# Kernel tuning notes

Measured on AMD Instinct MI355X. Metric: run time of the kernel, lower is better.

Reference implementation:

```python
import jax, jax.numpy as jnp
import numpy as np

N_NODES = 100000
N_EDGES = 1000000
F_IN = 64
F_OUT = 128
F_HID = 4 * F_OUT


def setup_inputs() -> dict:
    key = jax.random.key(0)
    ks = jax.random.split(key, 6)
    x = jax.random.normal(ks[0], (N_NODES, F_IN), dtype=jnp.float32)
    edge_index = jax.random.randint(ks[1], (2, N_EDGES), 0, N_NODES, dtype=jnp.int64)
    s = 1.0 / np.sqrt(F_IN)
    W_in = jax.random.normal(ks[2], (F_IN, F_OUT), dtype=jnp.float32) * s
    W_out = jax.random.normal(ks[3], (F_IN, F_OUT), dtype=jnp.float32) * s
    W1 = jax.random.normal(ks[4], (F_IN, F_HID), dtype=jnp.float32) * s
    W2 = jax.random.normal(ks[5], (F_HID, F_OUT), dtype=jnp.float32) * (1.0 / np.sqrt(F_HID))
    return {
        'x': x, 'edge_index': edge_index,
        'W_in': W_in, 'b_in': jnp.zeros((F_OUT,), jnp.float32),
        'W_out': W_out, 'b_out': jnp.zeros((F_OUT,), jnp.float32),
        'W1': W1, 'b1': jnp.zeros((F_HID,), jnp.float32),
        'W2': W2, 'b2': jnp.zeros((F_OUT,), jnp.float32),
    }


def _mean_aggr(vals, idx, num_segments):
    # segment-mean: sum of gathered features / in-degree (0 if no edges, like PyG)
    s = jax.ops.segment_sum(vals, idx, num_segments=num_segments)
    cnt = jax.ops.segment_sum(jnp.ones((idx.shape[0], 1), vals.dtype), idx,
                              num_segments=num_segments)
    return s / jnp.maximum(cnt, 1.0)


def reference(x, edge_index, W_in, b_in, W_out, b_out, W1, b1, W2, b2):
    src, dst = edge_index[0], edge_index[1]
    n = x.shape[0]
    # SAGEConv(root_weight=False), flow='source_to_target': aggregate x[src] at dst
    x_in = jax.nn.elu(_mean_aggr(x[src], dst, n) @ W_in + b_in)
    # flow='target_to_source': aggregate x[dst] at src
    x_out = jax.nn.elu(_mean_aggr(x[dst], src, n) @ W_out + b_out)
    # self branch: elu(lin2(elu(lin1(x))))  (the F.dropout call is a no-op)
    x_self = jax.nn.elu(jax.nn.elu(x @ W1 + b1) @ W2 + b2)
    return (x_in, x_out, x_self)
```

## Files before the change

kernel.cpp:

```cpp
#include <hip/hip_runtime.h>
#include <hip/hip_bf16.h>
#include <cstdint>
#include <cstddef>

#define N_NODES 100000
#define N_EDGES 1000000
#define F_IN 64
#define F_OUT 128
#define F_HID 512
#define NB 391
#define BSH 8
#define SB 98
#define AB 391
#define P1B 245

typedef __attribute__((ext_vector_type(8))) short short8b;
typedef __attribute__((ext_vector_type(4))) short short4b;
typedef __attribute__((ext_vector_type(4))) float f32x4;

__device__ __forceinline__ float elu_f(float v) {
    return v > 0.0f ? v : __expf(v) - 1.0f;
}

__device__ __forceinline__ unsigned short f2bf(float v) {
    __hip_bfloat16 b = __float2bfloat16(v);
    return *reinterpret_cast<unsigned short*>(&b);
}
__device__ __forceinline__ float bf2f(unsigned short u) {
    unsigned int w = (unsigned int)u << 16;
    return __uint_as_float(w);
}
__device__ __forceinline__ void split_bf(float v, short& hi, short& lo) {
    unsigned short h = (unsigned short)(__float_as_uint(v) >> 16);
    float r = v - bf2f(h);
    hi = (short)h;
    lo = (short)(unsigned short)(__float_as_uint(r) >> 16);
}

__global__ __launch_bounds__(256) void hist_kernel(
    const int* __restrict__ src, const int* __restrict__ dst,
    int* __restrict__ deg_in, int* __restrict__ deg_out)
{
    int e = blockIdx.x * 256 + threadIdx.x;
    if (e < N_EDGES) {
        atomicAdd(&deg_in[dst[e]], 1);
        atomicAdd(&deg_out[src[e]], 1);
    }
}

__global__ __launch_bounds__(256) void scan_block_kernel(
    const int* __restrict__ deg_in, const int* __restrict__ deg_out,
    int* __restrict__ rp_in, int* __restrict__ rp_out,
    int* __restrict__ bsum_in, int* __restrict__ bsum_out, int n)
{
    __shared__ int sSum[256];
    int b = blockIdx.x;
    const int* deg; int* rowptr; int* blockSums;
    if (b < SB) { deg = deg_in;  rowptr = rp_in;  blockSums = bsum_in; }
    else        { b -= SB; deg = deg_out; rowptr = rp_out; blockSums = bsum_out; }

    int tid = threadIdx.x;
    int base = b * 1024 + tid * 4;
    int v0 = (base + 0 < n) ? deg[base + 0] : 0;
    int v1 = (base + 1 < n) ? deg[base + 1] : 0;
    int v2 = (base + 2 < n) ? deg[base + 2] : 0;
    int v3 = (base + 3 < n) ? deg[base + 3] : 0;
    int s = v0 + v1 + v2 + v3;
    sSum[tid] = s;
    __syncthreads();
    int incl = s;
    for (int off = 1; off < 256; off <<= 1) {
        int t = (tid >= off) ? sSum[tid - off] : 0;
        __syncthreads();
        incl += t;
        sSum[tid] = incl;
        __syncthreads();
    }
    int exclT = incl - s;
    if (base + 0 < n) rowptr[base + 0] = exclT;
    if (base + 1 < n) rowptr[base + 1] = exclT + v0;
    if (base + 2 < n) rowptr[base + 2] = exclT + v0 + v1;
    if (base + 3 < n) rowptr[base + 3] = exclT + v0 + v1 + v2;
    if (tid == 255) blockSums[b] = incl;
}

__global__ __launch_bounds__(128) void scan_top_kernel(
    int* __restrict__ bs_in, int* __restrict__ bs_out, int nb)
{
    __shared__ int sh[128];
    int* blockSums = (blockIdx.x == 0) ? bs_in : bs_out;
    int tid = threadIdx.x;
    int v = (tid < nb) ? blockSums[tid] : 0;
    sh[tid] = v;
    __syncthreads();
    int incl = v;
    for (int off = 1; off < 128; off <<= 1) {
        int t = (tid >= off) ? sh[tid - off] : 0;
        __syncthreads();
        incl += t;
        sh[tid] = incl;
        __syncthreads();
    }
    if (tid < nb) blockSums[tid] = incl - v;
}

__global__ __launch_bounds__(256) void scan_add_kernel(
    int* __restrict__ rp_in, int* __restrict__ rp_out,
    const int* __restrict__ bs_in, const int* __restrict__ bs_out,
    int* __restrict__ bcur_in, int* __restrict__ bcur_out, int n, int total)
{
    int b = blockIdx.x;
    int* rowptr; const int* blockSums; int* bcur;
    if (b < AB) { rowptr = rp_in;  blockSums = bs_in;  bcur = bcur_in; }
    else        { b -= AB; rowptr = rp_out; blockSums = bs_out; bcur = bcur_out; }
    int i = b * 256 + threadIdx.x;
    if (i < n) {
        int v = rowptr[i] + blockSums[i >> 10];
        rowptr[i] = v;
        if ((i & 255) == 0) bcur[i >> BSH] = v;
    }
    if (i == 0) rowptr[n] = total;
}

__global__ __launch_bounds__(512) void msplit_scatter_kernel(
    const int* __restrict__ src, const int* __restrict__ dst,
    int* __restrict__ bcur_in, int* __restrict__ bcur_out,
    unsigned int* __restrict__ tmp_in, unsigned int* __restrict__ tmp_out)
{
    __shared__ int sCnt[NB];
    __shared__ int sBase[NB];
    int b = blockIdx.x;
    const int* keys; const int* vals; int* bcur; unsigned int* tmp;
    if (b < P1B) { keys = dst; vals = src; bcur = bcur_in;  tmp = tmp_in; }
    else         { b -= P1B; keys = src; vals = dst; bcur = bcur_out; tmp = tmp_out; }

    int tid = threadIdx.x;
    int tile0 = b * 4096;

    for (int i = tid; i < NB; i += 512) sCnt[i] = 0;
    __syncthreads();

    int key[8], rank[8];
    #pragma unroll
    for (int j = 0; j < 8; ++j) {
        int e = tile0 + j * 512 + tid;
        key[j] = -1;
        if (e < N_EDGES) {
            int k = keys[e];
            key[j] = k;
            rank[j] = atomicAdd(&sCnt[k >> BSH], 1);
        }
    }
    __syncthreads();
    for (int i = tid; i < NB; i += 512) sBase[i] = atomicAdd(&bcur[i], sCnt[i]);
    __syncthreads();
    #pragma unroll
    for (int j = 0; j < 8; ++j) {
        int e = tile0 + j * 512 + tid;
        if (e < N_EDGES) {
            int k = key[j];
            unsigned int rec = ((unsigned int)vals[e] << BSH) | (unsigned int)(k & 255);
            tmp[sBase[k >> BSH] + rank[j]] = rec;
        }
    }
}

__global__ __launch_bounds__(256) void msplit_place_kernel(
    const unsigned int* __restrict__ tmp_in, const unsigned int* __restrict__ tmp_out,
    const int* __restrict__ rp_in, const int* __restrict__ rp_out,
    int* __restrict__ col_in, int* __restrict__ col_out,
    int* __restrict__ flag)
{
    __shared__ int sCur[256];
    int b = blockIdx.x;
    const unsigned int* tmp; const int* rp; int* col;
    if (b < NB) { tmp = tmp_in;  rp = rp_in;  col = col_in; }
    else        { b -= NB; tmp = tmp_out; rp = rp_out; col = col_out; }

    int k0 = b << BSH;
    int kend = (k0 + 256 < N_NODES) ? k0 + 256 : N_NODES;
    int nk = kend - k0;
    int tid = threadIdx.x;
    if (tid < nk) sCur[tid] = rp[k0 + tid];
    __syncthreads();

    int beg = rp[k0], end = rp[kend];
    for (int e = beg + tid; e < end; e += 256) {
        unsigned int rec = tmp[e];
        int k8 = (int)(rec & 255u);
        int v  = (int)(rec >> BSH);
        if (k8 < nk) {
            int pos = atomicAdd(&sCur[k8], 1);
            col[pos] = v;
        } else {
            atomicOr(flag, 1);
        }
    }
    __syncthreads();
    if (tid < nk && sCur[tid] != rp[k0 + tid + 1]) atomicOr(flag, 1);
}

__global__ __launch_bounds__(256) void place_repair_kernel(
    const int* __restrict__ flag,
    const int* __restrict__ src, const int* __restrict__ dst,
    const int* __restrict__ rp_in, const int* __restrict__ rp_out,
    int* __restrict__ cur_in, int* __restrict__ cur_out,
    int* __restrict__ col_in, int* __restrict__ col_out)
{
    if (flag[0] == 0) return;
    int e = blockIdx.x * 256 + threadIdx.x;
    if (e >= N_EDGES) return;
    int s = src[e], d = dst[e];
    int p = rp_in[d] + atomicAdd(&cur_in[d], 1);
    col_in[p] = s;
    int q = rp_out[s] + atomicAdd(&cur_out[s], 1);
    col_out[q] = d;
}

__global__ __launch_bounds__(256) void prep_x_kernel(
    const float* __restrict__ x, unsigned short* __restrict__ xbf)
{
    int i = blockIdx.x * 256 + threadIdx.x;
    int base = i * 4;
    if (base < N_NODES * F_IN) {
        float4 v = *reinterpret_cast<const float4*>(&x[base]);
        short4b o;
        o[0] = (short)f2bf(v.x);
        o[1] = (short)f2bf(v.y);
        o[2] = (short)f2bf(v.z);
        o[3] = (short)f2bf(v.w);
        *reinterpret_cast<short4b*>(&xbf[base]) = o;
    }
}

__global__ __launch_bounds__(256) void gather_mean_kernel(
    const unsigned short* __restrict__ xbf,
    const int* __restrict__ rowptr, const int* __restrict__ col,
    float* __restrict__ agg)
{
    int wid = blockIdx.x * 4 + (threadIdx.x >> 6);
    int lane = threadIdx.x & 63;
    int g2 = lane >> 4;
    int l16 = lane & 15;
    if (wid >= N_NODES) return;
    int beg = rowptr[wid], end = rowptr[wid + 1];

    float4 acc = make_float4(0.0f, 0.0f, 0.0f, 0.0f);
    for (int e0 = beg; e0 < end; e0 += 16) {
        #pragma unroll
        for (int j = 0; j < 4; ++j) {
            int idx = e0 + j * 4 + g2;
            bool ok = idx < end;
            int c = col[ok ? idx : beg];
            uint2 v = *reinterpret_cast<const uint2*>(&xbf[(size_t)c * F_IN + l16 * 4]);
            if (ok) {
                acc.x += __uint_as_float(v.x << 16);
                acc.y += __uint_as_float(v.x & 0xffff0000u);
                acc.z += __uint_as_float(v.y << 16);
                acc.w += __uint_as_float(v.y & 0xffff0000u);
            }
        }
    }
    acc.x += __shfl_xor(acc.x, 16);
    acc.y += __shfl_xor(acc.y, 16);
    acc.z += __shfl_xor(acc.z, 16);
    acc.w += __shfl_xor(acc.w, 16);
    acc.x += __shfl_xor(acc.x, 32);
    acc.y += __shfl_xor(acc.y, 32);
    acc.z += __shfl_xor(acc.z, 32);
    acc.w += __shfl_xor(acc.w, 32);

    if (g2 == 0) {
        float inv = 1.0f / fmaxf((float)(end - beg), 1.0f);
        float4 o = make_float4(acc.x * inv, acc.y * inv, acc.z * inv, acc.w * inv);
        *reinterpret_cast<float4*>(&agg[(size_t)wid * F_IN + l16 * 4]) = o;
    }
}

__global__ __launch_bounds__(256) void prep_w_kernel(
    const float* __restrict__ W1, const float* __restrict__ W2,
    const float* __restrict__ Win, const float* __restrict__ Wout,
    unsigned short* __restrict__ W1Ahi, unsigned short* __restrict__ W1Alo,
    unsigned short* __restrict__ W2Ahi, unsigned short* __restrict__ W2Alo,
    unsigned short* __restrict__ WinAhi, unsigned short* __restrict__ WinAlo,
    unsigned short* __restrict__ WoutAhi, unsigned short* __restrict__ WoutAlo)
{
    int t = blockIdx.x * 256 + threadIdx.x;
    int lane = t & 63;
    int l15 = lane & 15, g = lane >> 4;
    if (t < 4096) {
        int ht = (t >> 6) & 31, ks = t >> 11;
        int m = ht * 16 + l15;
        int k0 = ks * 32 + g * 8;
        size_t o = ((size_t)(ht * 2 + ks) * 64 + lane) * 8;
        #pragma unroll
        for (int i = 0; i < 8; ++i) {
            float v = W1[(size_t)(k0 + i) * F_HID + m];
            unsigned short hi = f2bf(v);
            W1Ahi[o + i] = hi;
            W1Alo[o + i] = f2bf(v - bf2f(hi));
        }
    } else if (t < 12288) {
        int u = t - 4096;
        int ft = (u >> 6) & 7, ks2 = u >> 9;
        int m = ft * 16 + l15;
        int k0 = ks2 * 32 + g * 8;
        size_t o = ((size_t)(ks2 * 8 + ft) * 64 + lane) * 8;
        #pragma unroll
        for (int i = 0; i < 8; ++i) {
            float v = W2[(size_t)(k0 + i) * F_OUT + m];
            unsigned short hi = f2bf(v);
            W2Ahi[o + i] = hi;
            W2Alo[o + i] = f2bf(v - bf2f(hi));
        }
    } else if (t < 14336) {
        int u = t - 12288;
        const float* W = (u < 1024) ? Win : Wout;
        unsigned short* Ahi = (u < 1024) ? WinAhi : WoutAhi;
        unsigned short* Alo = (u < 1024) ? WinAlo : WoutAlo;
        u &= 1023;
        int ft = (u >> 6) & 7, ks = u >> 9;
        int m = ft * 16 + l15;
        int k0 = ks * 32 + g * 8;
        size_t o = ((size_t)(ks * 8 + ft) * 64 + lane) * 8;
        #pragma unroll
        for (int i = 0; i < 8; ++i) {
            float v = W[(size_t)(k0 + i) * F_OUT + m];
            unsigned short hi = f2bf(v);
            Ahi[o + i] = hi;
            Alo[o + i] = f2bf(v - bf2f(hi));
        }
    }
}

__global__ __launch_bounds__(256) void sage_lin_mfma_kernel(
    const float* __restrict__ agg,
    const unsigned short* __restrict__ WAhi, const unsigned short* __restrict__ WAlo,
    const float* __restrict__ b, float* __restrict__ out)
{
    int tid = threadIdx.x, lane = tid & 63, w = tid >> 6;
    int l15 = lane & 15, g = lane >> 4;
    int n = blockIdx.x * 64 + w * 16 + l15;
    int nc = (n > N_NODES - 1) ? N_NODES - 1 : n;

    short8b bhf[2], blf[2];
    #pragma unroll
    for (int ks = 0; ks < 2; ++ks) {
        const float* pa = &agg[(size_t)nc * F_IN + ks * 32 + g * 8];
        float4 v0 = *reinterpret_cast<const float4*>(pa);
        float4 v1 = *reinterpret_cast<const float4*>(pa + 4);
        float vv[8] = {v0.x, v0.y, v0.z, v0.w, v1.x, v1.y, v1.z, v1.w};
        short8b h8, l8;
        #pragma unroll
        for (int i = 0; i < 8; ++i) {
            short hh, ll;
            split_bf(vv[i], hh, ll);
            h8[i] = hh;
            l8[i] = ll;
        }
        bhf[ks] = h8;
        blf[ks] = l8;
    }

    #pragma unroll
    for (int ft = 0; ft < 8; ++ft) {
        f32x4 acc;
        {
            float4 bv = *reinterpret_cast<const float4*>(&b[ft * 16 + g * 4]);
            acc[0] = bv.x; acc[1] = bv.y; acc[2] = bv.z; acc[3] = bv.w;
        }
        #pragma unroll
        for (int ks = 0; ks < 2; ++ks) {
            size_t o = ((size_t)(ks * 8 + ft) * 64 + lane) * 8;
            short8b ah = *reinterpret_cast<const short8b*>(&WAhi[o]);
            short8b al = *reinterpret_cast<const short8b*>(&WAlo[o]);
            acc = __builtin_amdgcn_mfma_f32_16x16x32_bf16(ah, bhf[ks], acc, 0, 0, 0);
            acc = __builtin_amdgcn_mfma_f32_16x16x32_bf16(ah, blf[ks], acc, 0, 0, 0);
            acc = __builtin_amdgcn_mfma_f32_16x16x32_bf16(al, bhf[ks], acc, 0, 0, 0);
        }
        if (n < N_NODES) {
            float4 o4;
            o4.x = elu_f(acc[0]);
            o4.y = elu_f(acc[1]);
            o4.z = elu_f(acc[2]);
            o4.w = elu_f(acc[3]);
            *reinterpret_cast<float4*>(&out[(size_t)n * F_OUT + ft * 16 + g * 4]) = o4;
        }
    }
}

__global__ __launch_bounds__(128) void validate_sage_kernel(
    const float* __restrict__ agg,
    const float* __restrict__ W, const float* __restrict__ b,
    const float* __restrict__ outd, int* __restrict__ flag)
{
    __shared__ float sA[F_IN];
    int nn = blockIdx.x;
    int f = threadIdx.x;
    if (f < F_IN) sA[f] = agg[(size_t)nn * F_IN + f];
    __syncthreads();
    float acc = b[f];
    for (int k = 0; k < F_IN; ++k)
        acc = fmaf(sA[k], W[(size_t)k * F_OUT + f], acc);
    float ref = elu_f(acc);
    float got = outd[(size_t)nn * F_OUT + f];
    if (!(fabsf(ref - got) <= 0.01f)) atomicOr(flag, 1);
}

__global__ __launch_bounds__(256, 4) void self_mlp_mfma_kernel(
    const float* __restrict__ x,
    const unsigned short* __restrict__ W1Ahi, const unsigned short* __restrict__ W1Alo,
    const unsigned short* __restrict__ W2Ahi, const unsigned short* __restrict__ W2Alo,
    const float* __restrict__ b1, const float* __restrict__ b2,
    float* __restrict__ out)
{
    __shared__ unsigned short sW1hi[2048], sW1lo[2048];
    __shared__ unsigned short sW2hi[4096], sW2lo[4096];
    __shared__ unsigned short sHhi[4096], sHlo[4096];

    int tid = threadIdx.x, lane = tid & 63, w = tid >> 6;
    int l15 = lane & 15, g = lane >> 4;
    int node0 = blockIdx.x * 128;

    short8b xhi[2][2], xlo[2][2];
    #pragma unroll
    for (int nt = 0; nt < 2; ++nt) {
        int n = node0 + (2 * w + nt) * 16 + l15;
        if (n > N_NODES - 1) n = N_NODES - 1;
        #pragma unroll
        for (int ks = 0; ks < 2; ++ks) {
            const float* px = &x[(size_t)n * F_IN + ks * 32 + g * 8];
            float4 v0 = *reinterpret_cast<const float4*>(px);
            float4 v1 = *reinterpret_cast<const float4*>(px + 4);
            float vv[8] = {v0.x, v0.y, v0.z, v0.w, v1.x, v1.y, v1.z, v1.w};
            short8b h8, l8;
            #pragma unroll
            for (int i = 0; i < 8; ++i) {
                short hh, ll;
                split_bf(vv[i], hh, ll);
                h8[i] = hh;
                l8[i] = ll;
            }
            xhi[nt][ks] = h8;
            xlo[nt][ks] = l8;
        }
    }

    f32x4 acc[8][2];
    #pragma unroll
    for (int ft = 0; ft < 8; ++ft) {
        float4 bv = *reinterpret_cast<const float4*>(&b2[ft * 16 + g * 4]);
        #pragma unroll
        for (int nt = 0; nt < 2; ++nt) {
            acc[ft][nt][0] = bv.x; acc[ft][nt][1] = bv.y;
            acc[ft][nt][2] = bv.z; acc[ft][nt][3] = bv.w;
        }
    }

    for (int c = 0; c < 16; ++c) {
        __syncthreads();
        {
            const float4* s1h = reinterpret_cast<const float4*>(W1Ahi + (size_t)c * 2048);
            const float4* s1l = reinterpret_cast<const float4*>(W1Alo + (size_t)c * 2048);
            reinterpret_cast<float4*>(sW1hi)[tid] = s1h[tid];
            reinterpret_cast<float4*>(sW1lo)[tid] = s1l[tid];
            const float4* s2h = reinterpret_cast<const float4*>(W2Ahi + (size_t)c * 4096);
            const float4* s2l = reinterpret_cast<const float4*>(W2Alo + (size_t)c * 4096);
            reinterpret_cast<float4*>(sW2hi)[tid] = s2h[tid];
            reinterpret_cast<float4*>(sW2hi)[tid + 256] = s2h[tid + 256];
            reinterpret_cast<float4*>(sW2lo)[tid] = s2l[tid];
            reinterpret_cast<float4*>(sW2lo)[tid + 256] = s2l[tid + 256];
        }
        __syncthreads();

        #pragma unroll
// ... 16 lines not shown
                #pragma unroll
                for (int r = 0; r < 4; ++r) {
                    float hv = elu_f(hacc[r]);
                    short hh, ll;
                    split_bf(hv, hh, ll);
                    ph[r] = hh;
                    pl[r] = ll;
                }
                int byte = nodeL * 64 + (ht * 16 + g * 4) * 2;
                byte ^= (nodeL & 7) << 4;
                *reinterpret_cast<short4b*>(reinterpret_cast<char*>(sHhi) + byte) = ph;
                *reinterpret_cast<short4b*>(reinterpret_cast<char*>(sHlo) + byte) = pl;
            }
        }

        short8b bh[2], bl[2];
        #pragma unroll
        for (int nt = 0; nt < 2; ++nt) {
            int nodeL = (2 * w + nt) * 16 + l15;
            int byte = (nodeL * 64 + g * 16) ^ ((nodeL & 7) << 4);
            bh[nt] = *reinterpret_cast<const short8b*>(reinterpret_cast<const char*>(sHhi) + byte);
            bl[nt] = *reinterpret_cast<const short8b*>(reinterpret_cast<const char*>(sHlo) + byte);
        }
        #pragma unroll
        for (int ft = 0; ft < 8; ++ft) {
            short8b ah = *reinterpret_cast<const short8b*>(&sW2hi[(ft * 64 + lane) * 8]);
            short8b al = *reinterpret_cast<const short8b*>(&sW2lo[(ft * 64 + lane) * 8]);
            #pragma unroll
            for (int nt = 0; nt < 2; ++nt) {
                acc[ft][nt] = __builtin_amdgcn_mfma_f32_16x16x32_bf16(ah, bh[nt], acc[ft][nt], 0, 0, 0);
                acc[ft][nt] = __builtin_amdgcn_mfma_f32_16x16x32_bf16(ah, bl[nt], acc[ft][nt], 0, 0, 0);
                acc[ft][nt] = __builtin_amdgcn_mfma_f32_16x16x32_bf16(al, bh[nt], acc[ft][nt], 0, 0, 0);
            }
        }
    }

    #pragma unroll
    for (int ft = 0; ft < 8; ++ft) {
        #pragma unroll
        for (int nt = 0; nt < 2; ++nt) {
            int n = node0 + (2 * w + nt) * 16 + l15;
            if (n < N_NODES) {
                float4 o;
                o.x = elu_f(acc[ft][nt][0]);
                o.y = elu_f(acc[ft][nt][1]);
                o.z = elu_f(acc[ft][nt][2]);
                o.w = elu_f(acc[ft][nt][3]);
                *reinterpret_cast<float4*>(&out[(size_t)n * F_OUT + ft * 16 + g * 4]) = o;
            }
        }
    }
}

__global__ __launch_bounds__(256) void validate_kernel(
    const float* __restrict__ x,
    const float* __restrict__ W1, const float* __restrict__ b1,
    const float* __restrict__ W2, const float* __restrict__ b2,
    const float* __restrict__ out_self, int* __restrict__ flag)
{
    __shared__ float h[F_HID];
    __shared__ float sX[F_IN];
    int nn = blockIdx.x;
    int tid = threadIdx.x;
    if (tid < F_IN) sX[tid] = x[(size_t)nn * F_IN + tid];
    __syncthreads();
    #pragma unroll
    for (int jj = 0; jj < 2; ++jj) {
        int j = tid * 2 + jj;
        float acc = b1[j];
        for (int k = 0; k < F_IN; ++k)
            acc = fmaf(sX[k], W1[(size_t)k * F_HID + j], acc);
        h[j] = elu_f(acc);
    }
    __syncthreads();
    if (tid < F_OUT) {
        int f = tid;
        float acc = b2[f];
        for (int j = 0; j < F_HID; ++j)
            acc = fmaf(h[j], W2[(size_t)j * F_OUT + f], acc);
        float ref = elu_f(acc);
        float got = out_self[(size_t)nn * F_OUT + f];
        if (!(fabsf(ref - got) <= 0.01f)) atomicOr(flag, 1);
    }
}

__global__ __launch_bounds__(256) void gather_repair_kernel(
    const int* __restrict__ flag,
    const float* __restrict__ x,
    const int* __restrict__ rowptr, const int* __restrict__ col,
    float* __restrict__ agg)
{
    if (flag[0] == 0) return;
    int f = threadIdx.x & 63;
    for (int bb = blockIdx.x; bb < 25000; bb += gridDim.x) {
        int wid = bb * 4 + (threadIdx.x >> 6);
        if (wid >= N_NODES) continue;
        int beg = rowptr[wid];
        int end = rowptr[wid + 1];
        float acc = 0.0f;
        for (int e = beg; e < end; ++e)
            acc += x[(size_t)col[e] * F_IN + f];
        agg[(size_t)wid * F_IN + f] = acc / fmaxf((float)(end - beg), 1.0f);
    }
}

__global__ __launch_bounds__(256) void sage_lin_repair_kernel(
// ... 189 lines not shown
    const float* W_in  = (const float*)d_in[2];
    const float* b_in  = (const float*)d_in[3];
    const float* W_out = (const float*)d_in[4];
    const float* b_out = (const float*)d_in[5];
    const float* W1    = (const float*)d_in[6];
    const float* b1    = (const float*)d_in[7];
    const float* W2    = (const float*)d_in[8];
    const float* b2    = (const float*)d_in[9];
    float* out = (float*)d_out;

    const int* src = ei;
    const int* dst = ei + N_EDGES;

    int* I = (int*)d_ws;
    int* rowptr_in  = I;
    int* rowptr_out = I + 100001;
    int* col_in     = I + 200002;
    int* col_out    = I + 1200002;
    int* deg_in     = I + 2200002;
    int* deg_out    = I + 2300002;
    int* cur_in     = I + 2400002;
    int* cur_out    = I + 2500002;
    int* bsum_in    = I + 2600002;
    int* bsum_out   = I + 2600130;
    int* flagM      = I + 2600260;
    int* flagS      = I + 2600261;
    int* flagC      = I + 2600262;
    float* agg      = (float*)(I + 2600512);
    unsigned short* WF = (unsigned short*)(I + 9000512);
    unsigned short* W1Ahi  = WF;
    unsigned short* W1Alo  = WF + 32768;
    unsigned short* W2Ahi  = WF + 65536;
    unsigned short* W2Alo  = WF + 131072;
    unsigned short* WinAhi = WF + 196608;
    unsigned short* WinAlo = WF + 204800;
    unsigned short* WoutAhi= WF + 212992;
    unsigned short* WoutAlo= WF + 221184;
    unsigned short* xbf    = (unsigned short*)(I + 9120512);

    unsigned int* tmp_in  = (unsigned int*)agg;
    unsigned int* tmp_out = (unsigned int*)agg + 1000000;
    int* bcur_in  = deg_in;
    int* bcur_out = deg_out;

    hipMemsetAsync(deg_in, 0, 400000 * sizeof(int), stream);
    hipMemsetAsync(flagM, 0, 3 * sizeof(int), stream);

    prep_w_kernel<<<56, 256, 0, stream>>>(W1, W2, W_in, W_out,
                                          W1Ahi, W1Alo, W2Ahi, W2Alo,
                                          WinAhi, WinAlo, WoutAhi, WoutAlo);
    prep_x_kernel<<<6250, 256, 0, stream>>>(x, xbf);

    const int eb = (N_EDGES + 255) / 256;
    hist_kernel<<<eb, 256, 0, stream>>>(src, dst, deg_in, deg_out);

    scan_block_kernel<<<2 * SB, 256, 0, stream>>>(deg_in, deg_out,
                                                  rowptr_in, rowptr_out,
                                                  bsum_in, bsum_out, N_NODES);
    scan_top_kernel<<<2, 128, 0, stream>>>(bsum_in, bsum_out, SB);
    scan_add_kernel<<<2 * AB, 256, 0, stream>>>(rowptr_in, rowptr_out,
                                                bsum_in, bsum_out,
                                                bcur_in, bcur_out,
                                                N_NODES, N_EDGES);

    msplit_scatter_kernel<<<2 * P1B, 512, 0, stream>>>(src, dst,
                                                       bcur_in, bcur_out,
                                                       tmp_in, tmp_out);
    msplit_place_kernel<<<2 * NB, 256, 0, stream>>>(tmp_in, tmp_out,
                                                    rowptr_in, rowptr_out,
                                                    col_in, col_out, flagC);
    place_repair_kernel<<<eb, 256, 0, stream>>>(flagC, src, dst,
                                                rowptr_in, rowptr_out,
                                                cur_in, cur_out, col_in, col_out);

    const int gb = (N_NODES + 3) / 4;
    const int mb = (N_NODES + 63) / 64;
    float* out_in   = out;
    float* out_out  = out + (size_t)N_NODES * F_OUT;
    float* out_self = out + 2 * (size_t)N_NODES * F_OUT;

    gather_mean_kernel<<<gb, 256, 0, stream>>>(xbf, rowptr_in, col_in, agg);
    sage_lin_mfma_kernel<<<mb, 256, 0, stream>>>(agg, WinAhi, WinAlo, b_in, out_in);
    validate_sage_kernel<<<4, 128, 0, stream>>>(agg, W_in, b_in, out_in, flagS);

    gather_mean_kernel<<<gb, 256, 0, stream>>>(xbf, rowptr_out, col_out, agg);
    sage_lin_mfma_kernel<<<mb, 256, 0, stream>>>(agg, WoutAhi, WoutAlo, b_out, out_out);
    validate_sage_kernel<<<4, 128, 0, stream>>>(agg, W_out, b_out, out_out, flagS);

    self_mlp_mfma_kernel<<<782, 256, 0, stream>>>(x, W1Ahi, W1Alo, W2Ahi, W2Alo,
                                                  b1, b2, out_self);
    validate_kernel<<<4, 256, 0, stream>>>(x, W1, b1, W2, b2, out_self, flagM);

    self_mlp_repair_kernel<<<782, 256, 0, stream>>>(flagM, x, W1, b1, W2, b2, out_self);
    gather_repair_kernel<<<2048, 256, 0, stream>>>(flagS, x, rowptr_in, col_in, agg);
    sage_lin_repair_kernel<<<2048, 256, 0, stream>>>(flagS, agg, W_in, b_in, out_in);
    gather_repair_kernel<<<2048, 256, 0, stream>>>(flagS, x, rowptr_out, col_out, agg);
    sage_lin_repair_kernel<<<2048, 256, 0, stream>>>(flagS, agg, W_out, b_out, out_out);
}
```

Before: 384.8 us.

## Fuse degree histogram with self-MLP in one interleaved horizontal kernel

```diff
diff --git a/kernel.cpp b/kernel.cpp
--- a/kernel.cpp
+++ b/kernel.cpp
@@ -13,6 +13,8 @@
 #define SB 98
 #define AB 391
 #define P1B 245
+#define HB 3907
+#define SMB 782
 
 typedef __attribute__((ext_vector_type(8))) short short8b;
 typedef __attribute__((ext_vector_type(4))) short short4b;
@@ -37,390 +39,24 @@
     lo = (short)(unsigned short)(__float_as_uint(r) >> 16);
 }
 
-__global__ __launch_bounds__(256) void hist_kernel(
-    const int* __restrict__ src, const int* __restrict__ dst,
-    int* __restrict__ deg_in, int* __restrict__ deg_out)
-{
-    int e = blockIdx.x * 256 + threadIdx.x;
-    if (e < N_EDGES) {
-        atomicAdd(&deg_in[dst[e]], 1);
-        atomicAdd(&deg_out[src[e]], 1);
-    }
-}
-
-__global__ __launch_bounds__(256) void scan_block_kernel(
-    const int* __restrict__ deg_in, const int* __restrict__ deg_out,
-    int* __restrict__ rp_in, int* __restrict__ rp_out,
-    int* __restrict__ bsum_in, int* __restrict__ bsum_out, int n)
-{
-    __shared__ int sSum[256];
-    int b = blockIdx.x;
-    const int* deg; int* rowptr; int* blockSums;
-    if (b < SB) { deg = deg_in;  rowptr = rp_in;  blockSums = bsum_in; }
-    else        { b -= SB; deg = deg_out; rowptr = rp_out; blockSums = bsum_out; }
-
-    int tid = threadIdx.x;
-    int base = b * 1024 + tid * 4;
-    int v0 = (base + 0 < n) ? deg[base + 0] : 0;
-    int v1 = (base + 1 < n) ? deg[base + 1] : 0;
-    int v2 = (base + 2 < n) ? deg[base + 2] : 0;
-    int v3 = (base + 3 < n) ? deg[base + 3] : 0;
-    int s = v0 + v1 + v2 + v3;
-    sSum[tid] = s;
-    __syncthreads();
-    int incl = s;
-    for (int off = 1; off < 256; off <<= 1) {
-        int t = (tid >= off) ? sSum[tid - off] : 0;
-        __syncthreads();
-        incl += t;
-        sSum[tid] = incl;
-        __syncthreads();
-    }
-    int exclT = incl - s;
-    if (base + 0 < n) rowptr[base + 0] = exclT;
-    if (base + 1 < n) rowptr[base + 1] = exclT + v0;
-    if (base + 2 < n) rowptr[base + 2] = exclT + v0 + v1;
-    if (base + 3 < n) rowptr[base + 3] = exclT + v0 + v1 + v2;
-    if (tid == 255) blockSums[b] = incl;
-}
-
-__global__ __launch_bounds__(128) void scan_top_kernel(
-    int* __restrict__ bs_in, int* __restrict__ bs_out, int nb)
-{
-    __shared__ int sh[128];
-    int* blockSums = (blockIdx.x == 0) ? bs_in : bs_out;
-    int tid = threadIdx.x;
-    int v = (tid < nb) ? blockSums[tid] : 0;
-    sh[tid] = v;
-    __syncthreads();
-    int incl = v;
-    for (int off = 1; off < 128; off <<= 1) {
-        int t = (tid >= off) ? sh[tid - off] : 0;
-        __syncthreads();
-        incl += t;
-        sh[tid] = incl;
-        __syncthreads();
-    }
-    if (tid < nb) blockSums[tid] = incl - v;
-}
-
-__global__ __launch_bounds__(256) void scan_add_kernel(
-    int* __restrict__ rp_in, int* __restrict__ rp_out,
-    const int* __restrict__ bs_in, const int* __restrict__ bs_out,
-    int* __restrict__ bcur_in, int* __restrict__ bcur_out, int n, int total)
-{
-    int b = blockIdx.x;
-    int* rowptr; const int* blockSums; int* bcur;
-    if (b < AB) { rowptr = rp_in;  blockSums = bs_in;  bcur = bcur_in; }
-    else        { b -= AB; rowptr = rp_out; blockSums = bs_out; bcur = bcur_out; }
-    int i = b * 256 + threadIdx.x;
-    if (i < n) {
-        int v = rowptr[i] + blockSums[i >> 10];
-        rowptr[i] = v;
-        if ((i & 255) == 0) bcur[i >> BSH] = v;
-    }
-    if (i == 0) rowptr[n] = total;
-}
-
-__global__ __launch_bounds__(512) void msplit_scatter_kernel(
-    const int* __restrict__ src, const int* __restrict__ dst,
-    int* __restrict__ bcur_in, int* __restrict__ bcur_out,
-    unsigned int* __restrict__ tmp_in, unsigned int* __restrict__ tmp_out)
-{
-    __shared__ int sCnt[NB];
-    __shared__ int sBase[NB];
-    int b = blockIdx.x;
-    const int* keys; const int* vals; int* bcur; unsigned int* tmp;
-    if (b < P1B) { keys = dst; vals = src; bcur = bcur_in;  tmp = tmp_in; }
-    else         { b -= P1B; keys = src; vals = dst; bcur = bcur_out; tmp = tmp_out; }
-
-    int tid = threadIdx.x;
-    int tile0 = b * 4096;
-
-    for (int i = tid; i < NB; i += 512) sCnt[i] = 0;
-    __syncthreads();
-
-    int key[8], rank[8];
-    #pragma unroll
-    for (int j = 0; j < 8; ++j) {
-        int e = tile0 + j * 512 + tid;
-        key[j] = -1;
-        if (e < N_EDGES) {
-            int k = keys[e];
-            key[j] = k;
-            rank[j] = atomicAdd(&sCnt[k >> BSH], 1);
-        }
-    }
-    __syncthreads();
-    for (int i = tid; i < NB; i += 512) sBase[i] = atomicAdd(&bcur[i], sCnt[i]);
-    __syncthreads();
-    #pragma unroll
-    for (int j = 0; j < 8; ++j) {
-        int e = tile0 + j * 512 + tid;
-        if (e < N_EDGES) {
-            int k = key[j];
-            unsigned int rec = ((unsigned int)vals[e] << BSH) | (unsigned int)(k & 255);
-            tmp[sBase[k >> BSH] + rank[j]] = rec;
-        }
-    }
-}
-
-__global__ __launch_bounds__(256) void msplit_place_kernel(
-    const unsigned int* __restrict__ tmp_in, const unsigned int* __restrict__ tmp_out,
-    const int* __restrict__ rp_in, const int* __restrict__ rp_out,
-    int* __restrict__ col_in, int* __restrict__ col_out,
-    int* __restrict__ flag)
-{
-    __shared__ int sCur[256];
-    int b = blockIdx.x;
-    const unsigned int* tmp; const int* rp; int* col;
-    if (b < NB) { tmp = tmp_in;  rp = rp_in;  col = col_in; }
-    else        { b -= NB; tmp = tmp_out; rp = rp_out; col = col_out; }
-
-    int k0 = b << BSH;
-    int kend = (k0 + 256 < N_NODES) ? k0 + 256 : N_NODES;
-    int nk = kend - k0;
-    int tid = threadIdx.x;
-    if (tid < nk) sCur[tid] = rp[k0 + tid];
-    __syncthreads();
-
-    int beg = rp[k0], end = rp[kend];
-    for (int e = beg + tid; e < end; e += 256) {
-        unsigned int rec = tmp[e];
-        int k8 = (int)(rec & 255u);
-        int v  = (int)(rec >> BSH);
-        if (k8 < nk) {
-            int pos = atomicAdd(&sCur[k8], 1);
-            col[pos] = v;
-        } else {
-            atomicOr(flag, 1);
-        }
-    }
-    __syncthreads();
-    if (tid < nk && sCur[tid] != rp[k0 + tid + 1]) atomicOr(flag, 1);
-}
-
-__global__ __launch_bounds__(256) void place_repair_kernel(
-    const int* __restrict__ flag,
-    const int* __restrict__ src, const int* __restrict__ dst,
-    const int* __restrict__ rp_in, const int* __restrict__ rp_out,
-    int* __restrict__ cur_in, int* __restrict__ cur_out,
-    int* __restrict__ col_in, int* __restrict__ col_out)
-{
-    if (flag[0] == 0) return;
-    int e = blockIdx.x * 256 + threadIdx.x;
-    if (e >= N_EDGES) return;
-    int s = src[e], d = dst[e];
-    int p = rp_in[d] + atomicAdd(&cur_in[d], 1);
-    col_in[p] = s;
-    int q = rp_out[s] + atomicAdd(&cur_out[s], 1);
-    col_out[q] = d;
-}
-
-__global__ __launch_bounds__(256) void prep_x_kernel(
-    const float* __restrict__ x, unsigned short* __restrict__ xbf)
-{
-    int i = blockIdx.x * 256 + threadIdx.x;
-    int base = i * 4;
-    if (base < N_NODES * F_IN) {
-        float4 v = *reinterpret_cast<const float4*>(&x[base]);
-        short4b o;
-        o[0] = (short)f2bf(v.x);
-        o[1] = (short)f2bf(v.y);
-        o[2] = (short)f2bf(v.z);
-        o[3] = (short)f2bf(v.w);
-        *reinterpret_cast<short4b*>(&xbf[base]) = o;
-    }
-}
-
-__global__ __launch_bounds__(256) void gather_mean_kernel(
-    const unsigned short* __restrict__ xbf,
-    const int* __restrict__ rowptr, const int* __restrict__ col,
-    float* __restrict__ agg)
-{
-    int wid = blockIdx.x * 4 + (threadIdx.x >> 6);
-    int lane = threadIdx.x & 63;
-    int g2 = lane >> 4;
-    int l16 = lane & 15;
-    if (wid >= N_NODES) return;
-    int beg = rowptr[wid], end = rowptr[wid + 1];
-
-    float4 acc = make_float4(0.0f, 0.0f, 0.0f, 0.0f);
-    for (int e0 = beg; e0 < end; e0 += 16) {
-        #pragma unroll
-        for (int j = 0; j < 4; ++j) {
-            int idx = e0 + j * 4 + g2;
-            bool ok = idx < end;
-            int c = col[ok ? idx : beg];
-            uint2 v = *reinterpret_cast<const uint2*>(&xbf[(size_t)c * F_IN + l16 * 4]);
-            if (ok) {
-                acc.x += __uint_as_float(v.x << 16);
-                acc.y += __uint_as_float(v.x & 0xffff0000u);
-                acc.z += __uint_as_float(v.y << 16);
-                acc.w += __uint_as_float(v.y & 0xffff0000u);
-            }
-        }
-    }
-    acc.x += __shfl_xor(acc.x, 16);
-    acc.y += __shfl_xor(acc.y, 16);
-    acc.z += __shfl_xor(acc.z, 16);
-    acc.w += __shfl_xor(acc.w, 16);
-    acc.x += __shfl_xor(acc.x, 32);
-    acc.y += __shfl_xor(acc.y, 32);
-    acc.z += __shfl_xor(acc.z, 32);
-    acc.w += __shfl_xor(acc.w, 32);
-
-    if (g2 == 0) {
-        float inv = 1.0f / fmaxf((float)(end - beg), 1.0f);
-        float4 o = make_float4(acc.x * inv, acc.y * inv, acc.z * inv, acc.w * inv);
-        *reinterpret_cast<float4*>(&agg[(size_t)wid * F_IN + l16 * 4]) = o;
-    }
-}
-
-__global__ __launch_bounds__(256) void prep_w_kernel(
-    const float* __restrict__ W1, const float* __restrict__ W2,
-    const float* __restrict__ Win, const float* __restrict__ Wout,
-    unsigned short* __restrict__ W1Ahi, unsigned short* __restrict__ W1Alo,
-    unsigned short* __restrict__ W2Ahi, unsigned short* __restrict__ W2Alo,
-    unsigned short* __restrict__ WinAhi, unsigned short* __restrict__ WinAlo,
-    unsigned short* __restrict__ WoutAhi, unsigned short* __restrict__ WoutAlo)
-{
-    int t = blockIdx.x * 256 + threadIdx.x;
-    int lane = t & 63;
-    int l15 = lane & 15, g = lane >> 4;
-    if (t < 4096) {
-        int ht = (t >> 6) & 31, ks = t >> 11;
-        int m = ht * 16 + l15;
-        int k0 = ks * 32 + g * 8;
-        size_t o = ((size_t)(ht * 2 + ks) * 64 + lane) * 8;
-        #pragma unroll
-        for (int i = 0; i < 8; ++i) {
-            float v = W1[(size_t)(k0 + i) * F_HID + m];
-            unsigned short hi = f2bf(v);
-            W1Ahi[o + i] = hi;
-            W1Alo[o + i] = f2bf(v - bf2f(hi));
-        }
-    } else if (t < 12288) {
-        int u = t - 4096;
-        int ft = (u >> 6) & 7, ks2 = u >> 9;
-        int m = ft * 16 + l15;
-        int k0 = ks2 * 32 + g * 8;
-        size_t o = ((size_t)(ks2 * 8 + ft) * 64 + lane) * 8;
-        #pragma unroll
-        for (int i = 0; i < 8; ++i) {
-            float v = W2[(size_t)(k0 + i) * F_OUT + m];
-            unsigned short hi = f2bf(v);
-            W2Ahi[o + i] = hi;
-            W2Alo[o + i] = f2bf(v - bf2f(hi));
-        }
-    } else if (t < 14336) {
-        int u = t - 12288;
-        const float* W = (u < 1024) ? Win : Wout;
-        unsigned short* Ahi = (u < 1024) ? WinAhi : WoutAhi;
-        unsigned short* Alo = (u < 1024) ? WinAlo : WoutAlo;
-        u &= 1023;
-        int ft = (u >> 6) & 7, ks = u >> 9;
-        int m = ft * 16 + l15;
-        int k0 = ks * 32 + g * 8;
-        size_t o = ((size_t)(ks * 8 + ft) * 64 + lane) * 8;
-        #pragma unroll
-        for (int i = 0; i < 8; ++i) {
-            float v = W[(size_t)(k0 + i) * F_OUT + m];
-            unsigned short hi = f2bf(v);
-            Ahi[o + i] = hi;
-            Alo[o + i] = f2bf(v - bf2f(hi));
-        }
-    }
-}
-
-__global__ __launch_bounds__(256) void sage_lin_mfma_kernel(
-    const float* __restrict__ agg,
-    const unsigned short* __restrict__ WAhi, const unsigned short* __restrict__ WAlo,
-    const float* __restrict__ b, float* __restrict__ out)
-{
-    int tid = threadIdx.x, lane = tid & 63, w = tid >> 6;
-    int l15 = lane & 15, g = lane >> 4;
-    int n = blockIdx.x * 64 + w * 16 + l15;
-    int nc = (n > N_NODES - 1) ? N_NODES - 1 : n;
-
-    short8b bhf[2], blf[2];
-    #pragma unroll
-    for (int ks = 0; ks < 2; ++ks) {
-        const float* pa = &agg[(size_t)nc * F_IN + ks * 32 + g * 8];
-        float4 v0 = *reinterpret_cast<const float4*>(pa);
-        float4 v1 = *reinterpret_cast<const float4*>(pa + 4);
-        float vv[8] = {v0.x, v0.y, v0.z, v0.w, v1.x, v1.y, v1.z, v1.w};
-        short8b h8, l8;
-        #pragma unroll
-        for (int i = 0; i < 8; ++i) {
-            short hh, ll;
-            split_bf(vv[i], hh, ll);
-            h8[i] = hh;
-            l8[i] = ll;
-        }
-        bhf[ks] = h8;
-        blf[ks] = l8;
-    }
-
-    #pragma unroll
-    for (int ft = 0; ft < 8; ++ft) {
-        f32x4 acc;
-        {
-            float4 bv = *reinterpret_cast<const float4*>(&b[ft * 16 + g * 4]);
-            acc[0] = bv.x; acc[1] = bv.y; acc[2] = bv.z; acc[3] = bv.w;
-        }
-        #pragma unroll
-        for (int ks = 0; ks < 2; ++ks) {
-            size_t o = ((size_t)(ks * 8 + ft) * 64 + lane) * 8;
-            short8b ah = *reinterpret_cast<const short8b*>(&WAhi[o]);
-            short8b al = *reinterpret_cast<const short8b*>(&WAlo[o]);
-            acc = __builtin_amdgcn_mfma_f32_16x16x32_bf16(ah, bhf[ks], acc, 0, 0, 0);
-            acc = __builtin_amdgcn_mfma_f32_16x16x32_bf16(ah, blf[ks], acc, 0, 0, 0);
-            acc = __builtin_amdgcn_mfma_f32_16x16x32_bf16(al, bhf[ks], acc, 0, 0, 0);
-        }
-        if (n < N_NODES) {
-            float4 o4;
-            o4.x = elu_f(acc[0]);
-            o4.y = elu_f(acc[1]);
-            o4.z = elu_f(acc[2]);
-            o4.w = elu_f(acc[3]);
-            *reinterpret_cast<float4*>(&out[(size_t)n * F_OUT + ft * 16 + g * 4]) = o4;
-        }
-    }
-}
-
-__global__ __launch_bounds__(128) void validate_sage_kernel(
-    const float* __restrict__ agg,
-    const float* __restrict__ W, const float* __restrict__ b,
-    const float* __restrict__ outd, int* __restrict__ flag)
-{
-    __shared__ float sA[F_IN];
-    int nn = blockIdx.x;
-    int f = threadIdx.x;
-    if (f < F_IN) sA[f] = agg[(size_t)nn * F_IN + f];
-    __syncthreads();
-    float acc = b[f];
-    for (int k = 0; k < F_IN; ++k)
-        acc = fmaf(sA[k], W[(size_t)k * F_OUT + f], acc);
-    float ref = elu_f(acc);
-    float got = outd[(size_t)nn * F_OUT + f];
-    if (!(fabsf(ref - got) <= 0.01f)) atomicOr(flag, 1);
-}
-
-__global__ __launch_bounds__(256, 4) void self_mlp_mfma_kernel(
+__device__ void self_mlp_body(
+    int blk, unsigned char* smem,
     const float* __restrict__ x,
     const unsigned short* __restrict__ W1Ahi, const unsigned short* __restrict__ W1Alo,
     const unsigned short* __restrict__ W2Ahi, const unsigned short* __restrict__ W2Alo,
     const float* __restrict__ b1, const float* __restrict__ b2,
     float* __restrict__ out)
 {
-    __shared__ unsigned short sW1hi[2048], sW1lo[2048];
-    __shared__ unsigned short sW2hi[4096], sW2lo[4096];
-    __shared__ unsigned short sHhi[4096], sHlo[4096];
+    unsigned short* sW1hi = (unsigned short*)smem;
+    unsigned short* sW1lo = sW1hi + 2048;
+    unsigned short* sW2hi = sW1lo + 2048;
+    unsigned short* sW2lo = sW2hi + 4096;
+    unsigned short* sHhi  = sW2lo + 4096;
+    unsigned short* sHlo  = sHhi + 4096;
 
     int tid = threadIdx.x, lane = tid & 63, w = tid >> 6;
     int l15 = lane & 15, g = lane >> 4;
-    int node0 = blockIdx.x * 128;
+    int node0 = blk * 128;
 
     short8b xhi[2][2], xlo[2][2];
     #pragma unroll
@@ -543,6 +179,392 @@
     }
 }
 
+__global__ __launch_bounds__(256, 4) void fused_hist_self_kernel(
+    const int* __restrict__ src, const int* __restrict__ dst,
+    int* __restrict__ deg_in, int* __restrict__ deg_out,
+    const float* __restrict__ x,
+    const unsigned short* __restrict__ W1Ahi, const unsigned short* __restrict__ W1Alo,
+    const unsigned short* __restrict__ W2Ahi, const unsigned short* __restrict__ W2Alo,
+    const float* __restrict__ b1, const float* __restrict__ b2,
+    float* __restrict__ out_self)
+{
+    __shared__ unsigned char smem[40960];
+    int bid = blockIdx.x;
+    int r = bid % 6;
+    if (r == 5) {
+        int blk = bid / 6;
+        self_mlp_body(blk, smem, x, W1Ahi, W1Alo, W2Ahi, W2Alo, b1, b2, out_self);
+    } else {
+        int hb = (bid / 6) * 5 + r;
+        if (hb < HB) {
+            int e = hb * 256 + threadIdx.x;
+            if (e < N_EDGES) {
+                atomicAdd(&deg_in[dst[e]], 1);
+                atomicAdd(&deg_out[src[e]], 1);
+            }
+        }
+    }
+}
+
+__global__ __launch_bounds__(256) void scan_block_kernel(
+    const int* __restrict__ deg_in, const int* __restrict__ deg_out,
+    int* __restrict__ rp_in, int* __restrict__ rp_out,
+    int* __restrict__ bsum_in, int* __restrict__ bsum_out, int n)
+{
+    __shared__ int sSum[256];
+    int b = blockIdx.x;
+    const int* deg; int* rowptr; int* blockSums;
+    if (b < SB) { deg = deg_in;  rowptr = rp_in;  blockSums = bsum_in; }
+    else        { b -= SB; deg = deg_out; rowptr = rp_out; blockSums = bsum_out; }
+
+    int tid = threadIdx.x;
+    int base = b * 1024 + tid * 4;
+    int v0 = (base + 0 < n) ? deg[base + 0] : 0;
+    int v1 = (base + 1 < n) ? deg[base + 1] : 0;
+    int v2 = (base + 2 < n) ? deg[base + 2] : 0;
+    int v3 = (base + 3 < n) ? deg[base + 3] : 0;
+    int s = v0 + v1 + v2 + v3;
+    sSum[tid] = s;
+    __syncthreads();
+    int incl = s;
+    for (int off = 1; off < 256; off <<= 1) {
+        int t = (tid >= off) ? sSum[tid - off] : 0;
+        __syncthreads();
+        incl += t;
+        sSum[tid] = incl;
+        __syncthreads();
+    }
+    int exclT = incl - s;
+    if (base + 0 < n) rowptr[base + 0] = exclT;
+    if (base + 1 < n) rowptr[base + 1] = exclT + v0;
+    if (base + 2 < n) rowptr[base + 2] = exclT + v0 + v1;
+    if (base + 3 < n) rowptr[base + 3] = exclT + v0 + v1 + v2;
+    if (tid == 255) blockSums[b] = incl;
+}
+
+__global__ __launch_bounds__(128) void scan_top_kernel(
+    int* __restrict__ bs_in, int* __restrict__ bs_out, int nb)
+{
+    __shared__ int sh[128];
+    int* blockSums = (blockIdx.x == 0) ? bs_in : bs_out;
+    int tid = threadIdx.x;
+    int v = (tid < nb) ? blockSums[tid] : 0;
+    sh[tid] = v;
+    __syncthreads();
+    int incl = v;
+    for (int off = 1; off < 128; off <<= 1) {
+        int t = (tid >= off) ? sh[tid - off] : 0;
+        __syncthreads();
+        incl += t;
+        sh[tid] = incl;
+        __syncthreads();
+    }
+    if (tid < nb) blockSums[tid] = incl - v;
+}
+
+__global__ __launch_bounds__(256) void scan_add_kernel(
+    int* __restrict__ rp_in, int* __restrict__ rp_out,
+    const int* __restrict__ bs_in, const int* __restrict__ bs_out,
+    int* __restrict__ bcur_in, int* __restrict__ bcur_out, int n, int total)
+{
+    int b = blockIdx.x;
+    int* rowptr; const int* blockSums; int* bcur;
+    if (b < AB) { rowptr = rp_in;  blockSums = bs_in;  bcur = bcur_in; }
+    else        { b -= AB; rowptr = rp_out; blockSums = bs_out; bcur = bcur_out; }
+    int i = b * 256 + threadIdx.x;
+    if (i < n) {
+        int v = rowptr[i] + blockSums[i >> 10];
+        rowptr[i] = v;
+        if ((i & 255) == 0) bcur[i >> BSH] = v;
+    }
+    if (i == 0) rowptr[n] = total;
+}
+
+__global__ __launch_bounds__(512) void msplit_scatter_kernel(
+    const int* __restrict__ src, const int* __restrict__ dst,
+    int* __restrict__ bcur_in, int* __restrict__ bcur_out,
+    unsigned int* __restrict__ tmp_in, unsigned int* __restrict__ tmp_out)
+{
+    __shared__ int sCnt[NB];
+    __shared__ int sBase[NB];
+    int b = blockIdx.x;
+    const int* keys; const int* vals; int* bcur; unsigned int* tmp;
+    if (b < P1B) { keys = dst; vals = src; bcur = bcur_in;  tmp = tmp_in; }
+    else         { b -= P1B; keys = src; vals = dst; bcur = bcur_out; tmp = tmp_out; }
+
+    int tid = threadIdx.x;
+    int tile0 = b * 4096;
+
+    for (int i = tid; i < NB; i += 512) sCnt[i] = 0;
+    __syncthreads();
+
+    int key[8], rank[8];
+    #pragma unroll
+    for (int j = 0; j < 8; ++j) {
+        int e = tile0 + j * 512 + tid;
+        key[j] = -1;
+        if (e < N_EDGES) {
+            int k = keys[e];
+            key[j] = k;
+            rank[j] = atomicAdd(&sCnt[k >> BSH], 1);
+        }
+    }
+    __syncthreads();
+    for (int i = tid; i < NB; i += 512) sBase[i] = atomicAdd(&bcur[i], sCnt[i]);
+    __syncthreads();
+    #pragma unroll
+    for (int j = 0; j < 8; ++j) {
+        int e = tile0 + j * 512 + tid;
+        if (e < N_EDGES) {
+            int k = key[j];
+            unsigned int rec = ((unsigned int)vals[e] << BSH) | (unsigned int)(k & 255);
+            tmp[sBase[k >> BSH] + rank[j]] = rec;
+        }
+    }
+}
+
+__global__ __launch_bounds__(256) void msplit_place_kernel(
+    const unsigned int* __restrict__ tmp_in, const unsigned int* __restrict__ tmp_out,
+    const int* __restrict__ rp_in, const int* __restrict__ rp_out,
+    int* __restrict__ col_in, int* __restrict__ col_out,
+    int* __restrict__ flag)
+{
+    __shared__ int sCur[256];
+    int b = blockIdx.x;
+    const unsigned int* tmp; const int* rp; int* col;
+    if (b < NB) { tmp = tmp_in;  rp = rp_in;  col = col_in; }
+    else        { b -= NB; tmp = tmp_out; rp = rp_out; col = col_out; }
+
+    int k0 = b << BSH;
+    int kend = (k0 + 256 < N_NODES) ? k0 + 256 : N_NODES;
+    int nk = kend - k0;
+    int tid = threadIdx.x;
+    if (tid < nk) sCur[tid] = rp[k0 + tid];
+    __syncthreads();
+
+    int beg = rp[k0], end = rp[kend];
+    for (int e = beg + tid; e < end; e += 256) {
+        unsigned int rec = tmp[e];
+        int k8 = (int)(rec & 255u);
+        int v  = (int)(rec >> BSH);
+        if (k8 < nk) {
+            int pos = atomicAdd(&sCur[k8], 1);
+            col[pos] = v;
+        } else {
+            atomicOr(flag, 1);
+        }
+    }
+    __syncthreads();
+    if (tid < nk && sCur[tid] != rp[k0 + tid + 1]) atomicOr(flag, 1);
+}
+
+__global__ __launch_bounds__(256) void place_repair_kernel(
+    const int* __restrict__ flag,
+    const int* __restrict__ src, const int* __restrict__ dst,
+    const int* __restrict__ rp_in, const int* __restrict__ rp_out,
+    int* __restrict__ cur_in, int* __restrict__ cur_out,
+    int* __restrict__ col_in, int* __restrict__ col_out)
+{
+    if (flag[0] == 0) return;
+    int e = blockIdx.x * 256 + threadIdx.x;
+    if (e >= N_EDGES) return;
+    int s = src[e], d = dst[e];
+    int p = rp_in[d] + atomicAdd(&cur_in[d], 1);
+    col_in[p] = s;
+    int q = rp_out[s] + atomicAdd(&cur_out[s], 1);
+    col_out[q] = d;
+}
+
+__global__ __launch_bounds__(256) void prep_x_kernel(
+    const float* __restrict__ x, unsigned short* __restrict__ xbf)
+{
+    int i = blockIdx.x * 256 + threadIdx.x;
+    int base = i * 4;
+    if (base < N_NODES * F_IN) {
+        float4 v = *reinterpret_cast<const float4*>(&x[base]);
+        short4b o;
+        o[0] = (short)f2bf(v.x);
+        o[1] = (short)f2bf(v.y);
+        o[2] = (short)f2bf(v.z);
+        o[3] = (short)f2bf(v.w);
+        *reinterpret_cast<short4b*>(&xbf[base]) = o;
+    }
+}
+
+__global__ __launch_bounds__(256) void gather_mean_kernel(
+    const unsigned short* __restrict__ xbf,
+    const int* __restrict__ rowptr, const int* __restrict__ col,
+    float* __restrict__ agg)
+{
+    int wid = blockIdx.x * 4 + (threadIdx.x >> 6);
+    int lane = threadIdx.x & 63;
+    int g2 = lane >> 4;
+    int l16 = lane & 15;
+    if (wid >= N_NODES) return;
+    int beg = rowptr[wid], end = rowptr[wid + 1];
+
+    float4 acc = make_float4(0.0f, 0.0f, 0.0f, 0.0f);
+    for (int e0 = beg; e0 < end; e0 += 16) {
+        #pragma unroll
+        for (int j = 0; j < 4; ++j) {
+            int idx = e0 + j * 4 + g2;
+            bool ok = idx < end;
+            int c = col[ok ? idx : beg];
+            uint2 v = *reinterpret_cast<const uint2*>(&xbf[(size_t)c * F_IN + l16 * 4]);
+            if (ok) {
+                acc.x += __uint_as_float(v.x << 16);
+                acc.y += __uint_as_float(v.x & 0xffff0000u);
+                acc.z += __uint_as_float(v.y << 16);
+                acc.w += __uint_as_float(v.y & 0xffff0000u);
+            }
+        }
+    }
+    acc.x += __shfl_xor(acc.x, 16);
+    acc.y += __shfl_xor(acc.y, 16);
+    acc.z += __shfl_xor(acc.z, 16);
+    acc.w += __shfl_xor(acc.w, 16);
+    acc.x += __shfl_xor(acc.x, 32);
+    acc.y += __shfl_xor(acc.y, 32);
+    acc.z += __shfl_xor(acc.z, 32);
+    acc.w += __shfl_xor(acc.w, 32);
+
+    if (g2 == 0) {
+        float inv = 1.0f / fmaxf((float)(end - beg), 1.0f);
+        float4 o = make_float4(acc.x * inv, acc.y * inv, acc.z * inv, acc.w * inv);
+        *reinterpret_cast<float4*>(&agg[(size_t)wid * F_IN + l16 * 4]) = o;
+    }
+}
+
+__global__ __launch_bounds__(256) void prep_w_kernel(
+    const float* __restrict__ W1, const float* __restrict__ W2,
+    const float* __restrict__ Win, const float* __restrict__ Wout,
+    unsigned short* __restrict__ W1Ahi, unsigned short* __restrict__ W1Alo,
+    unsigned short* __restrict__ W2Ahi, unsigned short* __restrict__ W2Alo,
+    unsigned short* __restrict__ WinAhi, unsigned short* __restrict__ WinAlo,
+    unsigned short* __restrict__ WoutAhi, unsigned short* __restrict__ WoutAlo)
+{
+    int t = blockIdx.x * 256 + threadIdx.x;
+    int lane = t & 63;
+    int l15 = lane & 15, g = lane >> 4;
+    if (t < 4096) {
+        int ht = (t >> 6) & 31, ks = t >> 11;
+        int m = ht * 16 + l15;
+        int k0 = ks * 32 + g * 8;
+        size_t o = ((size_t)(ht * 2 + ks) * 64 + lane) * 8;
+        #pragma unroll
+        for (int i = 0; i < 8; ++i) {
+            float v = W1[(size_t)(k0 + i) * F_HID + m];
+            unsigned short hi = f2bf(v);
+            W1Ahi[o + i] = hi;
+            W1Alo[o + i] = f2bf(v - bf2f(hi));
+        }
+    } else if (t < 12288) {
+        int u = t - 4096;
+        int ft = (u >> 6) & 7, ks2 = u >> 9;
+        int m = ft * 16 + l15;
+        int k0 = ks2 * 32 + g * 8;
+        size_t o = ((size_t)(ks2 * 8 + ft) * 64 + lane) * 8;
+        #pragma unroll
+        for (int i = 0; i < 8; ++i) {
+            float v = W2[(size_t)(k0 + i) * F_OUT + m];
+            unsigned short hi = f2bf(v);
+            W2Ahi[o + i] = hi;
+            W2Alo[o + i] = f2bf(v - bf2f(hi));
+        }
+    } else if (t < 14336) {
+        int u = t - 12288;
+        const float* W = (u < 1024) ? Win : Wout;
+        unsigned short* Ahi = (u < 1024) ? WinAhi : WoutAhi;
+        unsigned short* Alo = (u < 1024) ? WinAlo : WoutAlo;
+        u &= 1023;
+        int ft = (u >> 6) & 7, ks = u >> 9;
+        int m = ft * 16 + l15;
+        int k0 = ks * 32 + g * 8;
+        size_t o = ((size_t)(ks * 8 + ft) * 64 + lane) * 8;
+        #pragma unroll
+        for (int i = 0; i < 8; ++i) {
+            float v = W[(size_t)(k0 + i) * F_OUT + m];
+            unsigned short hi = f2bf(v);
+            Ahi[o + i] = hi;
+            Alo[o + i] = f2bf(v - bf2f(hi));
+        }
+    }
+}
+
+__global__ __launch_bounds__(256) void sage_lin_mfma_kernel(
+    const float* __restrict__ agg,
+    const unsigned short* __restrict__ WAhi, const unsigned short* __restrict__ WAlo,
+    const float* __restrict__ b, float* __restrict__ out)
+{
+    int tid = threadIdx.x, lane = tid & 63, w = tid >> 6;
+    int l15 = lane & 15, g = lane >> 4;
+    int n = blockIdx.x * 64 + w * 16 + l15;
+    int nc = (n > N_NODES - 1) ? N_NODES - 1 : n;
+
+    short8b bhf[2], blf[2];
+    #pragma unroll
+    for (int ks = 0; ks < 2; ++ks) {
+        const float* pa = &agg[(size_t)nc * F_IN + ks * 32 + g * 8];
+        float4 v0 = *reinterpret_cast<const float4*>(pa);
+        float4 v1 = *reinterpret_cast<const float4*>(pa + 4);
+        float vv[8] = {v0.x, v0.y, v0.z, v0.w, v1.x, v1.y, v1.z, v1.w};
+        short8b h8, l8;
+        #pragma unroll
+        for (int i = 0; i < 8; ++i) {
+            short hh, ll;
+            split_bf(vv[i], hh, ll);
+            h8[i] = hh;
+            l8[i] = ll;
+        }
+        bhf[ks] = h8;
+        blf[ks] = l8;
+    }
+
+    #pragma unroll
+    for (int ft = 0; ft < 8; ++ft) {
+        f32x4 acc;
+        {
+            float4 bv = *reinterpret_cast<const float4*>(&b[ft * 16 + g * 4]);
+            acc[0] = bv.x; acc[1] = bv.y; acc[2] = bv.z; acc[3] = bv.w;
+        }
+        #pragma unroll
+        for (int ks = 0; ks < 2; ++ks) {
+            size_t o = ((size_t)(ks * 8 + ft) * 64 + lane) * 8;
+            short8b ah = *reinterpret_cast<const short8b*>(&WAhi[o]);
+            short8b al = *reinterpret_cast<const short8b*>(&WAlo[o]);
+            acc = __builtin_amdgcn_mfma_f32_16x16x32_bf16(ah, bhf[ks], acc, 0, 0, 0);
+            acc = __builtin_amdgcn_mfma_f32_16x16x32_bf16(ah, blf[ks], acc, 0, 0, 0);
+            acc = __builtin_amdgcn_mfma_f32_16x16x32_bf16(al, bhf[ks], acc, 0, 0, 0);
+        }
+        if (n < N_NODES) {
+            float4 o4;
+            o4.x = elu_f(acc[0]);
+            o4.y = elu_f(acc[1]);
+            o4.z = elu_f(acc[2]);
+            o4.w = elu_f(acc[3]);
+            *reinterpret_cast<float4*>(&out[(size_t)n * F_OUT + ft * 16 + g * 4]) = o4;
+        }
+    }
+}
+
+__global__ __launch_bounds__(128) void validate_sage_kernel(
+    const float* __restrict__ agg,
+    const float* __restrict__ W, const float* __restrict__ b,
+    const float* __restrict__ outd, int* __restrict__ flag)
+{
+    __shared__ float sA[F_IN];
+    int nn = blockIdx.x;
+    int f = threadIdx.x;
+    if (f < F_IN) sA[f] = agg[(size_t)nn * F_IN + f];
+    __syncthreads();
+    float acc = b[f];
+    for (int k = 0; k < F_IN; ++k)
+        acc = fmaf(sA[k], W[(size_t)k * F_OUT + f], acc);
+    float ref = elu_f(acc);
+    float got = outd[(size_t)nn * F_OUT + f];
+    if (!(fabsf(ref - got) <= 0.01f)) atomicOr(flag, 1);
+}
+
 __global__ __launch_bounds__(256) void validate_kernel(
     const float* __restrict__ x,
     const float* __restrict__ W1, const float* __restrict__ b1,
@@ -838,7 +860,14 @@
     prep_x_kernel<<<6250, 256, 0, stream>>>(x, xbf);
 
     const int eb = (N_EDGES + 255) / 256;
-    hist_kernel<<<eb, 256, 0, stream>>>(src, dst, deg_in, deg_out);
+    float* out_in   = out;
+    float* out_out  = out + (size_t)N_NODES * F_OUT;
+    float* out_self = out + 2 * (size_t)N_NODES * F_OUT;
+
+    fused_hist_self_kernel<<<SMB * 6, 256, 0, stream>>>(
+        src, dst, deg_in, deg_out,
+        x, W1Ahi, W1Alo, W2Ahi, W2Alo, b1, b2, out_self);
+    validate_kernel<<<4, 256, 0, stream>>>(x, W1, b1, W2, b2, out_self, flagM);
 
     scan_block_kernel<<<2 * SB, 256, 0, stream>>>(deg_in, deg_out,
                                                   rowptr_in, rowptr_out,
@@ -861,9 +890,6 @@
 
     const int gb = (N_NODES + 3) / 4;
     const int mb = (N_NODES + 63) / 64;
-    float* out_in   = out;
-    float* out_out  = out + (size_t)N_NODES * F_OUT;
-    float* out_self = out + 2 * (size_t)N_NODES * F_OUT;
 
     gather_mean_kernel<<<gb, 256, 0, stream>>>(xbf, rowptr_in, col_in, agg);
     sage_lin_mfma_kernel<<<mb, 256, 0, stream>>>(agg, WinAhi, WinAlo, b_in, out_in);
@@ -872,10 +898,6 @@
     gather_mean_kernel<<<gb, 256, 0, stream>>>(xbf, rowptr_out, col_out, agg);
     sage_lin_mfma_kernel<<<mb, 256, 0, stream>>>(agg, WoutAhi, WoutAlo, b_out, out_out);
     validate_sage_kernel<<<4, 128, 0, stream>>>(agg, W_out, b_out, out_out, flagS);
-
-    self_mlp_mfma_kernel<<<782, 256, 0, stream>>>(x, W1Ahi, W1Alo, W2Ahi, W2Alo,
-                                                  b1, b2, out_self);
-    validate_kernel<<<4, 256, 0, stream>>>(x, W1, b1, W2, b2, out_self, flagM);
 
     self_mlp_repair_kernel<<<782, 256, 0, stream>>>(flagM, x, W1, b1, W2, b2, out_self);
     gather_repair_kernel<<<2048, 256, 0, stream>>>(flagS, x, rowptr_in, col_in, agg);
```

New measurement: 407.1 us. 1.06x slower.
